# Kernel optimization log

Hardware: AMD Instinct MI355X
Metric: run time of the kernel (lower is better)

## Reference

```python
import jax, jax.numpy as jnp
import numpy as np

B, T, C, H = 4, 2048, 1024, 16
HS = C // H  # head dim = 64
EPS = 1e-5


def _layernorm(h, w, b):
    m = jnp.mean(h, axis=-1, keepdims=True)
    v = jnp.mean(jnp.square(h - m), axis=-1, keepdims=True)
    return (h - m) * jax.lax.rsqrt(v + EPS) * w + b


def _quantize_int8(t):
    # per-tensor absmax int8 quantization, matching the torch code
    absmax = jnp.max(jnp.abs(t))
    scale = jnp.where(absmax > 0, absmax / 127.0, jnp.float32(1.0))
    q = jnp.clip(jnp.round(t / scale), -127, 127).astype(jnp.int8)
    return q, scale


def setup_inputs() -> dict:
    key = jax.random.key(0)
    ks = jax.random.split(key, 8)
    w = lambda k, shape: (jax.random.normal(k, shape, jnp.float32) * 0.02)
    return {
        "x": jax.random.normal(ks[0], (B, T, C), jnp.float32),
        "ln1_w": jnp.ones((C,), jnp.float32),
        "ln1_b": jnp.zeros((C,), jnp.float32),
        "W_qkv": w(ks[1], (C, 3 * C)),
        "b_qkv": jnp.zeros((3 * C,), jnp.float32),
        "W_o": w(ks[2], (C, C)),
        "b_o": jnp.zeros((C,), jnp.float32),
        "ln2_w": jnp.ones((C,), jnp.float32),
        "ln2_b": jnp.zeros((C,), jnp.float32),
        "W_fc": w(ks[3], (C, 4 * C)),
        "b_fc": jnp.zeros((4 * C,), jnp.float32),
        "W_pr": w(ks[4], (4 * C, C)),
        "b_pr": jnp.zeros((C,), jnp.float32),
    }


def reference(x, ln1_w, ln1_b, W_qkv, b_qkv, W_o, b_o, ln2_w, ln2_b, W_fc, b_fc, W_pr, b_pr):
    # ---- attention (prefill, cache-owner, kv_cache_quant=True, use_cache=True) ----
    h = _layernorm(x, ln1_w, ln1_b)
    qkv = h @ W_qkv + b_qkv                       # (B,T,3C)
    q, k, v = jnp.split(qkv, 3, axis=-1)
    q = q.reshape(B, T, H, HS).transpose(0, 2, 1, 3)  # (B,H,T,hs)
    k = k.reshape(B, T, H, HS).transpose(0, 2, 1, 3)
    v = v.reshape(B, T, H, HS).transpose(0, 2, 1, 3)

    # quantized `present` cache (returned, not used for attention in prefill path)
    k_quant, k_scale = _quantize_int8(k)
    v_quant, v_scale = _quantize_int8(v)

    # causal SDPA (dropout=0)
    att = jnp.einsum("bhqd,bhkd->bhqk", q, k) * (1.0 / np.sqrt(HS))
    causal = jnp.tril(jnp.ones((T, T), bool))
    att = jnp.where(causal[None, None], att, jnp.float32(-jnp.inf))
    att = jax.nn.softmax(att, axis=-1)
    y = jnp.einsum("bhqk,bhkd->bhqd", att, v)
    y = y.transpose(0, 2, 1, 3).reshape(B, T, C)
    y = y @ W_o + b_o
    x = x + y

    # ---- MLP ----
    h2 = _layernorm(x, ln2_w, ln2_b)
    h2 = jax.nn.gelu(h2 @ W_fc + b_fc, approximate=False)
    x = x + (h2 @ W_pr + b_pr)

    return x, k_quant, k_scale, v_quant, v_scale
```

## Files before the change

kernel.cpp:

```cpp
#include <hip/hip_runtime.h>
#include <cmath>

typedef __bf16 bf16;
typedef float f32x4 __attribute__((ext_vector_type(4)));
typedef __bf16 bf16x4 __attribute__((ext_vector_type(4)));
typedef __bf16 bf16x8 __attribute__((ext_vector_type(8)));

#define DEVI __device__ __forceinline__

constexpr int Bn = 4, Tn = 2048, Cn = 1024, Hn = 16, HSn = 64;
constexpr int C3n = 3 * Cn;
constexpr int BTn = Bn * Tn;

constexpr size_t OFF_WT_QKV = 0;
constexpr size_t OFF_WT_O   = 6291456;
constexpr size_t OFF_WT_FC  = 8388608;
constexpr size_t OFF_WT_PR  = 16777216;
constexpr size_t OFF_H      = 25165824;
constexpr size_t OFF_Y      = 41943040;
constexpr size_t OFF_X1     = 58720256;
constexpr size_t OFF_AMAX   = 92274688;
constexpr size_t OFF_QKV    = 92274944;
constexpr size_t OFF_G      = OFF_QKV;

constexpr size_t OUT_X  = 0;
constexpr size_t OUT_KQ = 8388608;
constexpr size_t OUT_KS = 16777216;
constexpr size_t OUT_VQ = 16777217;
constexpr size_t OUT_VS = 25165825;

DEVI void g2l16(const void* g, void* l) {
  __builtin_amdgcn_global_load_lds(
      (__attribute__((address_space(1))) void*)g,
      (__attribute__((address_space(3))) void*)l, 16, 0, 0);
}

DEVI float gelu_f(float x) {
  const float ax = fabsf(x) * 0.7071067811865476f;
  const float t = 1.0f / (1.0f + 0.3275911f * ax);
  const float p = t * (0.254829592f + t * (-0.284496736f +
                  t * (1.421413741f + t * (-1.453152027f + t * 1.061405429f))));
  float er = 1.0f - p * __expf(-ax * ax);
  er = (x < 0.0f) ? -er : er;
  return 0.5f * x * (1.0f + er);
}

__global__ __launch_bounds__(256) void k_transpose(const float* __restrict__ W,
                                                   bf16* __restrict__ Wt,
                                                   int K, int N) {
  __shared__ float tile[32][33];
  const int n0 = blockIdx.x * 32, k0 = blockIdx.y * 32;
  const int tx = threadIdx.x, ty = threadIdx.y;
#pragma unroll
  for (int i = 0; i < 4; ++i) {
    int k = k0 + ty + i * 8;
    tile[ty + i * 8][tx] = W[(size_t)k * N + (n0 + tx)];
  }
  __syncthreads();
#pragma unroll
  for (int i = 0; i < 4; ++i) {
    int n = n0 + ty + i * 8;
    Wt[(size_t)n * K + (k0 + tx)] = (bf16)tile[tx][ty + i * 8];
  }
}

__global__ __launch_bounds__(256) void k_ln(const float* __restrict__ x,
                                            const float* __restrict__ g,
                                            const float* __restrict__ b,
                                            bf16* __restrict__ out) {
  __shared__ float red[8];
  const int row = blockIdx.x, tid = threadIdx.x;
  const int lane = tid & 63, wv = tid >> 6;
  f32x4 v = ((const f32x4*)(x + (size_t)row * Cn))[tid];

  float s = v[0] + v[1] + v[2] + v[3];
  s += __shfl_down(s, 32); s += __shfl_down(s, 16); s += __shfl_down(s, 8);
  s += __shfl_down(s, 4);  s += __shfl_down(s, 2);  s += __shfl_down(s, 1);
  if (!lane) red[wv] = s;
  __syncthreads();
  const float mean = (red[0] + red[1] + red[2] + red[3]) * (1.0f / 1024.0f);
  __syncthreads();

  f32x4 d = v - mean;
  float s2 = d[0]*d[0] + d[1]*d[1] + d[2]*d[2] + d[3]*d[3];
  s2 += __shfl_down(s2, 32); s2 += __shfl_down(s2, 16); s2 += __shfl_down(s2, 8);
  s2 += __shfl_down(s2, 4);  s2 += __shfl_down(s2, 2);  s2 += __shfl_down(s2, 1);
  if (!lane) red[wv] = s2;
  __syncthreads();
  const float var = (red[0] + red[1] + red[2] + red[3]) * (1.0f / 1024.0f);
  const float inv = rsqrtf(var + 1e-5f);

  f32x4 gw = ((const f32x4*)g)[tid];
  f32x4 bb = ((const f32x4*)b)[tid];
  bf16x4 o;
#pragma unroll
  for (int j = 0; j < 4; ++j) o[j] = (bf16)(d[j] * inv * gw[j] + bb[j]);
  *(bf16x4*)(out + (size_t)row * Cn + tid * 4) = o;
}

#define VMCNT(N) asm volatile("s_waitcnt vmcnt(" #N ")" ::: "memory")
#define LGKM0()  asm volatile("s_waitcnt lgkmcnt(0)" ::: "memory")
#define BARW()   asm volatile("s_barrier" ::: "memory")
#define SCHEDB() __builtin_amdgcn_sched_barrier(0)

DEVI void stage_half(const bf16* __restrict__ G, int ldk, int row0, int k0,
                     bf16* dst, int w, int lane) {
  const int srow = lane >> 3;
  const int sch = ((lane & 7) ^ srow) * 8;
  const bf16* src = G + (size_t)(row0 + srow) * ldk + k0 + sch;
#pragma unroll
  for (int i = 0; i < 2; ++i) {
    const int g = 2 * w + i;
    g2l16(src + (size_t)(8 * g) * ldk, dst + g * 512);
  }
}

DEVI void read_b(const bf16* BsB, int wn, int l15, int quad, bf16x8 (&bv)[2][2]) {
#pragma unroll
  for (int nt = 0; nt < 2; ++nt)
#pragma unroll
    for (int kk = 0; kk < 2; ++kk) {
      const int row = wn * 32 + nt * 16 + l15;
      const int c = ((kk * 4 + quad) ^ (l15 & 7)) * 8;
      bv[nt][kk] = *(const bf16x8*)(BsB + row * 64 + c);
    }
}

template <int Q>
DEVI void read_aq(const bf16* AsB, int wm, int l15, int quad, bf16x8 (&af)[2]) {
#pragma unroll
  for (int kk = 0; kk < 2; ++kk) {
    const int row = wm * 64 + Q * 16 + l15;
    const int c = ((kk * 4 + quad) ^ (l15 & 7)) * 8;
    af[kk] = *(const bf16x8*)(AsB + row * 64 + c);
  }
}

template <int Q>
DEVI void mfma_q(const bf16x8 (&af)[2], const bf16x8 (&bv)[2][2],
                 f32x4 (&acc)[4][2]) {
  __builtin_amdgcn_s_setprio(1);
#pragma unroll
  for (int nt = 0; nt < 2; ++nt)
#pragma unroll
    for (int kk = 0; kk < 2; ++kk)
      acc[Q][nt] = __builtin_amdgcn_mfma_f32_16x16x32_bf16(
          af[kk], bv[nt][kk], acc[Q][nt], 0, 0, 0);
  __builtin_amdgcn_s_setprio(0);
}

template <int BUF>
DEVI void tile_iter(int kt, int kIters, const bf16* __restrict__ A,
                    const bf16* __restrict__ Bt, int K, int m0, int n0,
                    bf16* As0, bf16* As1, bf16* Bs0, bf16* Bs1,
                    f32x4 (&acc)[4][2], int w, int lane) {
  const int l15 = lane & 15, quad = lane >> 4;
  const int wm = w >> 2, wn = w & 3;
  const bf16* AsB = BUF ? As1 : As0;
  const bf16* BsB = BUF ? Bs1 : Bs0;
  bf16* AsW = BUF ? As1 : As0;
  bf16* BsW = BUF ? Bs1 : Bs0;

  bf16x8 bv[2][2];
  bf16x8 af0[2], af1[2], af2[2], af3[2];

  read_b(BsB, wn, l15, quad, bv);
  read_aq<0>(AsB, wm, l15, quad, af0);
  read_aq<1>(AsB, wm, l15, quad, af1);
  LGKM0(); SCHEDB();
  mfma_q<0>(af0, bv, acc);
  SCHEDB();

  read_aq<2>(AsB, wm, l15, quad, af2);
  read_aq<3>(AsB, wm, l15, quad, af3);
  LGKM0(); SCHEDB();
  mfma_q<1>(af1, bv, acc);
  SCHEDB();
  BARW();

  if (kt + 2 < kIters) {
    stage_half(A,  K, m0, (kt + 2) * 64, AsW, w, lane);
    stage_half(Bt, K, n0, (kt + 2) * 64, BsW, w, lane);
  }
  mfma_q<2>(af2, bv, acc);
  mfma_q<3>(af3, bv, acc);
  SCHEDB();
  if (kt + 2 < kIters) {
    VMCNT(4);
    BARW();
  } else if (kt + 1 < kIters) {
    VMCNT(0);
    BARW();
  }
}

template <bool RES, bool GELU, bool AMAX, bool F32OUT>
__global__ __launch_bounds__(512, 4) void k_gemmT(const bf16* __restrict__ A,
                                                  const bf16* __restrict__ Bt,
                                                  const float* __restrict__ bias,
                                                  const float* __restrict__ res,
                                                  void* __restrict__ Cout,
                                                  unsigned int* __restrict__ amax,
                                                  int M, int N, int K) {
  __shared__ bf16 As0[128 * 64], As1[128 * 64];
  __shared__ bf16 Bs0[128 * 64], Bs1[128 * 64];
  __shared__ float redA[8];
  const int tid = threadIdx.x;
  const int lane = tid & 63, w = tid >> 6;
  const int wm = w >> 2, wn = w & 3;
  const int l15 = lane & 15, quad = lane >> 4;
  const int m0 = blockIdx.x * 128, n0 = blockIdx.y * 128;
  const int kIters = K >> 6;
  (void)M;

  stage_half(A,  K, m0, 0,  As0, w, lane);
  stage_half(Bt, K, n0, 0,  Bs0, w, lane);
  stage_half(A,  K, m0, 64, As1, w, lane);
  stage_half(Bt, K, n0, 64, Bs1, w, lane);
  VMCNT(4);
  BARW();

  f32x4 acc[4][2] = {};

  const int nPairs = kIters >> 1;
  for (int p = 0; p < nPairs; ++p) {
    tile_iter<0>(2 * p,     kIters, A, Bt, K, m0, n0, As0, As1, Bs0, Bs1, acc, w, lane);
    tile_iter<1>(2 * p + 1, kIters, A, Bt, K, m0, n0, As0, As1, Bs0, Bs1, acc, w, lane);
  }

  const int colB = n0 + wn * 32 + l15;
  const int rowB = m0 + wm * 64 + (quad << 2);
  float lm = 0.0f;
#pragma unroll
  for (int mt = 0; mt < 4; ++mt) {
#pragma unroll
    for (int nt = 0; nt < 2; ++nt) {
      const int col = colB + nt * 16;
      const float bval = bias[col];
#pragma unroll
      for (int r = 0; r < 4; ++r) {
        const int row = rowB + mt * 16 + r;
        float val = acc[mt][nt][r] + bval;
        if (GELU) val = gelu_f(val);
        if (RES)  val += res[(size_t)row * N + col];
        if (AMAX) lm = fmaxf(lm, fabsf(val));
        if (F32OUT) ((float*)Cout)[(size_t)row * N + col] = val;
        else        ((bf16*)Cout)[(size_t)row * N + col] = (bf16)val;
      }
    }
  }

  if (AMAX) {
    const int cls = n0 >> 10;
    if (cls > 0) {
      lm = fmaxf(lm, __shfl_xor(lm, 1));
      lm = fmaxf(lm, __shfl_xor(lm, 2));
      lm = fmaxf(lm, __shfl_xor(lm, 4));
      lm = fmaxf(lm, __shfl_xor(lm, 8));
      lm = fmaxf(lm, __shfl_xor(lm, 16));
      lm = fmaxf(lm, __shfl_xor(lm, 32));
      if (!lane) redA[w] = lm;
      __syncthreads();
      if (tid == 0) {
        float m8 = redA[0];
#pragma unroll
        for (int i = 1; i < 8; ++i) m8 = fmaxf(m8, redA[i]);
        atomicMax(amax + (cls - 1), __float_as_uint(m8));
      }
    }
  }
}

__global__ __launch_bounds__(256) void k_init(unsigned int* amax) {
  if (threadIdx.x < 2) amax[threadIdx.x] = 0u;
}

__global__ __launch_bounds__(256) void k_quant(const bf16* __restrict__ qkv,
                                               const unsigned int* __restrict__ amax,
                                               float* __restrict__ out) {
  const float ka = __uint_as_float(amax[0]);
  const float va = __uint_as_float(amax[1]);
  const float ks = ka > 0.0f ? ka / 127.0f : 1.0f;
  const float vs = va > 0.0f ? va / 127.0f : 1.0f;
  if (blockIdx.x == 0 && threadIdx.x == 0) { out[OUT_KS] = ks; out[OUT_VS] = vs; }
  const float kinv = 1.0f / ks, vinv = 1.0f / vs;
  const size_t nchunks = 1048576;
  const size_t stride = (size_t)gridDim.x * blockDim.x;
  for (size_t ci = (size_t)blockIdx.x * blockDim.x + threadIdx.x; ci < nchunks; ci += stride) {
    const int d0 = (int)(ci & 7) * 8;
    const int t  = (int)(ci >> 3) & 2047;
    const int h  = (int)(ci >> 14) & 15;
    const int b  = (int)(ci >> 18);
    const size_t src = ((size_t)(b * Tn + t)) * C3n + h * HSn + d0;
    bf16x8 k8 = *(const bf16x8*)(qkv + src + Cn);
    bf16x8 v8 = *(const bf16x8*)(qkv + src + 2 * Cn);
    float kq[8], vq[8];
#pragma unroll
    for (int j = 0; j < 8; ++j) {
      kq[j] = fminf(fmaxf(rintf((float)k8[j] * kinv), -127.0f), 127.0f);
      vq[j] = fminf(fmaxf(rintf((float)v8[j] * vinv), -127.0f), 127.0f);
    }
    const size_t oi = ci * 8;
    f32x4 a0 = {kq[0], kq[1], kq[2], kq[3]};
    f32x4 a1 = {kq[4], kq[5], kq[6], kq[7]};
    *(f32x4*)(out + OUT_KQ + oi)     = a0;
    *(f32x4*)(out + OUT_KQ + oi + 4) = a1;
    float* vdst = out + OUT_VQ + oi;
#pragma unroll
    for (int j = 0; j < 8; ++j) vdst[j] = vq[j];
  }
}

__global__ __launch_bounds__(256, 3) void k_attn(const bf16* __restrict__ qkv,
                                                 bf16* __restrict__ y) {
  __shared__ bf16 Ks[2][64 * 64];
  __shared__ bf16 Vt[2][64 * 64];
  __shared__ bf16 Pt[4][2][16 * 64];

  const int tid = threadIdx.x;
  const int lane = tid & 63;
  const int w = tid >> 6;
  const int quad = lane >> 4;
  const int l15 = lane & 15;

  const int bh = blockIdx.x;
  const int qt = 15 - (int)blockIdx.y;
  const int b = bh >> 4, h = bh & 15;
  const int q0 = qt * 128;
  const int ktMax = 2 * qt + 1;

  const bf16* qkv_b = qkv + (size_t)b * Tn * C3n + h * HSn;
  const bf16* kbase = qkv_b + Cn;
  const bf16* vbase = qkv_b + 2 * Cn;

  const int srow = lane >> 3;
  const int schunk = ((lane & 7) ^ srow) * 8;

  const bf16* q0p = qkv_b + (size_t)(q0 + 16 * w + l15) * C3n;
  const bf16* q1p = q0p + (size_t)64 * C3n;
  bf16x8 qf[2][2];
  qf[0][0] = *(const bf16x8*)(q0p + quad * 8);
  qf[0][1] = *(const bf16x8*)(q0p + 32 + quad * 8);
  qf[1][0] = *(const bf16x8*)(q1p + quad * 8);
  qf[1][1] = *(const bf16x8*)(q1p + 32 + quad * 8);

  g2l16(kbase + (size_t)(8 * w + srow) * C3n + schunk, (bf16*)Ks[0] + w * 512);
  g2l16(kbase + (size_t)(8 * (w + 4) + srow) * C3n + schunk, (bf16*)Ks[0] + (w + 4) * 512);
  bf16x8 v0 = *(const bf16x8*)(vbase + (size_t)lane * C3n + w * 8);
  bf16x8 v1 = *(const bf16x8*)(vbase + (size_t)lane * C3n + (w + 4) * 8);
  __builtin_amdgcn_s_waitcnt(0);
#pragma unroll
  for (int j = 0; j < 8; ++j) {
    Vt[0][(w * 8 + j) * 64 + ((srow ^ j) << 3) + (lane & 7)] = v0[j];
    Vt[0][((w + 4) * 8 + j) * 64 + ((srow ^ j) << 3) + (lane & 7)] = v1[j];
  }
  __syncthreads();

  f32x4 Od[2][4] = {};
  float m_i[2] = {-INFINITY, -INFINITY};
  float l_i[2] = {0.0f, 0.0f};

  for (int kt = 0; kt <= ktMax; ++kt) {
    const int bsel = kt & 1;

    bf16x8 nv0, nv1;
    if (kt < ktMax) {
      const int kv1 = (kt + 1) * 64;
      g2l16(kbase + (size_t)(kv1 + 8 * w + srow) * C3n + schunk,
            (bf16*)Ks[bsel ^ 1] + w * 512);
      g2l16(kbase + (size_t)(kv1 + 8 * (w + 4) + srow) * C3n + schunk,
            (bf16*)Ks[bsel ^ 1] + (w + 4) * 512);
      nv0 = *(const bf16x8*)(vbase + (size_t)(kv1 + lane) * C3n + w * 8);
      nv1 = *(const bf16x8*)(vbase + (size_t)(kv1 + lane) * C3n + (w + 4) * 8);
    }

    const bf16* KsB = Ks[bsel];
    f32x4 S0[4] = {}, S1[4] = {};
#pragma unroll
    for (int ks = 0; ks < 2; ++ks)
#pragma unroll
      for (int nt = 0; nt < 4; ++nt) {
        const int rn = nt * 16 + l15;
        const int c = ((ks * 4 + quad) ^ (l15 & 7)) * 8;
        bf16x8 kf = *(const bf16x8*)(KsB + rn * 64 + c);
        S0[nt] = __builtin_amdgcn_mfma_f32_16x16x32_bf16(kf, qf[0][ks], S0[nt], 0, 0, 0);
        S1[nt] = __builtin_amdgcn_mfma_f32_16x16x32_bf16(kf, qf[1][ks], S1[nt], 0, 0, 0);
      }

    const int qloc = 16 * w + l15;
    const int th[2] = { kt < 2 * qt ? 64 : (kt == 2 * qt ? qloc : -1),
                        kt < ktMax ? 64 : qloc };
    f32x4* Sg[2] = {S0, S1};
#pragma unroll
    for (int g = 0; g < 2; ++g) {
      float s[4][4];
      float mx = -INFINITY;
#pragma unroll
      for (int nt = 0; nt < 4; ++nt)
#pragma unroll
        for (int r = 0; r < 4; ++r) {
          float v = Sg[g][nt][r] * 0.125f;
          if (nt * 16 + quad * 4 + r > th[g]) v = -INFINITY;
          s[nt][r] = v;
          mx = fmaxf(mx, v);
        }
      mx = fmaxf(mx, __shfl_xor(mx, 16));
      mx = fmaxf(mx, __shfl_xor(mx, 32));
      const float mn = fmaxf(m_i[g], mx);
      const float al = __expf(m_i[g] - mn);
      m_i[g] = mn;
      float rsum = 0.0f;
      bf16x4 pk[4];
#pragma unroll
      for (int nt = 0; nt < 4; ++nt)
#pragma unroll
        for (int r = 0; r < 4; ++r) {
          const float p = __expf(s[nt][r] - mn);
          rsum += p;
          pk[nt][r] = (bf16)p;
        }
      rsum += __shfl_xor(rsum, 16);
      rsum += __shfl_xor(rsum, 32);
      l_i[g] = l_i[g] * al + rsum;
#pragma unroll
      for (int dt = 0; dt < 4; ++dt) Od[g][dt] *= al;
#pragma unroll
      for (int nt = 0; nt < 4; ++nt) {
        const int phys = (nt * 2 + (quad >> 1)) ^ (l15 & 7);
        *(bf16x4*)(&Pt[w][g][0] + l15 * 64 + phys * 8 + (quad & 1) * 4) = pk[nt];
      }
    }

    const bf16* VtB = Vt[bsel];
#pragma unroll
    for (int ks2 = 0; ks2 < 2; ++ks2) {
      const int pc = ((ks2 * 4 + quad) ^ (l15 & 7)) * 8;
      bf16x8 pf0 = *(const bf16x8*)(&Pt[w][0][0] + l15 * 64 + pc);
      bf16x8 pf1 = *(const bf16x8*)(&Pt[w][1][0] + l15 * 64 + pc);
#pragma unroll
      for (int dt = 0; dt < 4; ++dt) {
        const int d = dt * 16 + l15;
        bf16x8 vf = *(const bf16x8*)(VtB + d * 64 + pc);
        Od[0][dt] = __builtin_amdgcn_mfma_f32_16x16x32_bf16(vf, pf0, Od[0][dt], 0, 0, 0);
        Od[1][dt] = __builtin_amdgcn_mfma_f32_16x16x32_bf16(vf, pf1, Od[1][dt], 0, 0, 0);
      }
    }

    if (kt < ktMax) {
      __builtin_amdgcn_s_waitcnt(0);
#pragma unroll
      for (int j = 0; j < 8; ++j) {
        Vt[bsel ^ 1][(w * 8 + j) * 64 + ((srow ^ j) << 3) + (lane & 7)] = nv0[j];
        Vt[bsel ^ 1][((w + 4) * 8 + j) * 64 + ((srow ^ j) << 3) + (lane & 7)] = nv1[j];
      }
      __syncthreads();
    }
  }

#pragma unroll
  for (int g = 0; g < 2; ++g) {
    const float invl = 1.0f / l_i[g];
    const size_t yb = ((size_t)b * Tn + q0 + g * 64 + 16 * w + l15) * Cn + h * HSn;
#pragma unroll
    for (int dt = 0; dt < 4; ++dt) {
      bf16x4 o;
#pragma unroll
      for (int r = 0; r < 4; ++r) o[r] = (bf16)(Od[g][dt][r] * invl);
      *(bf16x4*)(y + yb + dt * 16 + quad * 4) = o;
    }
  }
}

extern "C" void kernel_launch(void* const* d_in, const int* in_sizes, int n_in,
                              void* d_out, int out_size, void* d_ws, size_t ws_size,
                              hipStream_t stream) {
  const float* x     = (const float*)d_in[0];
  const float* ln1w  = (const float*)d_in[1];
  const float* ln1b  = (const float*)d_in[2];
  const float* Wqkv  = (const float*)d_in[3];
  const float* bqkv  = (const float*)d_in[4];
  const float* Wo    = (const float*)d_in[5];
  const float* bo    = (const float*)d_in[6];
  const float* ln2w  = (const float*)d_in[7];
  const float* ln2b  = (const float*)d_in[8];
  const float* Wfc   = (const float*)d_in[9];
  const float* bfc   = (const float*)d_in[10];
  const float* Wpr   = (const float*)d_in[11];
  const float* bpr   = (const float*)d_in[12];

  char* ws = (char*)d_ws;
  bf16*  Wt_qkv = (bf16*)(ws + OFF_WT_QKV);
  bf16*  Wt_o   = (bf16*)(ws + OFF_WT_O);
  bf16*  Wt_fc  = (bf16*)(ws + OFF_WT_FC);
  bf16*  Wt_pr  = (bf16*)(ws + OFF_WT_PR);
  bf16*  h      = (bf16*)(ws + OFF_H);
  bf16*  ybf    = (bf16*)(ws + OFF_Y);
  float* x1     = (float*)(ws + OFF_X1);
  unsigned int* amax = (unsigned int*)(ws + OFF_AMAX);
  bf16*  qkvbf  = (bf16*)(ws + OFF_QKV);
  bf16*  g      = (bf16*)(ws + OFF_G);
  float* out    = (float*)d_out;

  const dim3 tb(32, 8);
  k_transpose<<<dim3(96, 32),  tb, 0, stream>>>(Wqkv, Wt_qkv, 1024, 3072);
  k_transpose<<<dim3(32, 32),  tb, 0, stream>>>(Wo,   Wt_o,   1024, 1024);
  k_transpose<<<dim3(128, 32), tb, 0, stream>>>(Wfc,  Wt_fc,  1024, 4096);
  k_transpose<<<dim3(32, 128), tb, 0, stream>>>(Wpr,  Wt_pr,  4096, 1024);
  k_init<<<1, 64, 0, stream>>>(amax);

  k_ln<<<BTn, 256, 0, stream>>>(x, ln1w, ln1b, h);
  k_gemmT<false, false, true, false><<<dim3(64, 24), 512, 0, stream>>>(
      h, Wt_qkv, bqkv, nullptr, qkvbf, amax, 8192, 3072, 1024);
  k_quant<<<2048, 256, 0, stream>>>(qkvbf, amax, out);
  k_attn<<<dim3(64, 16), 256, 0, stream>>>(qkvbf, ybf);
  k_gemmT<true, false, false, true><<<dim3(64, 8), 512, 0, stream>>>(
      ybf, Wt_o, bo, x, x1, nullptr, 8192, 1024, 1024);
  k_ln<<<BTn, 256, 0, stream>>>(x1, ln2w, ln2b, h);
  k_gemmT<false, true, false, false><<<dim3(64, 32), 512, 0, stream>>>(
      h, Wt_fc, bfc, nullptr, g, nullptr, 8192, 4096, 1024);
  k_gemmT<true, false, false, true><<<dim3(64, 8), 512, 0, stream>>>(
      g, Wt_pr, bpr, x1, out, nullptr, 8192, 1024, 4096);
}
```

Baseline: 527.1 us.

## Merge weight transposes and amax init into one launch; relax GEMM MFMA scheduling

The four weight-transpose kernels and the amax-init kernel become one k_prep launch that picks each block's job by block index, removing four launches and the small gaps between them. Separately, the GEMM inner loop loses its sched_barrier fences, the s_setprio raise around MFMA groups and the intermediate lgkmcnt wait. All four A fragments are now read before any MFMA and the compiler schedules freely. This may raise register pressure or lose the hand-tuned overlap of LDS reads with MFMAs.

```diff
diff --git a/kernel.cpp b/kernel.cpp
--- a/kernel.cpp
+++ b/kernel.cpp
@@ -45,11 +45,24 @@
   return 0.5f * x * (1.0f + er);
 }
 
-__global__ __launch_bounds__(256) void k_transpose(const float* __restrict__ W,
-                                                   bf16* __restrict__ Wt,
-                                                   int K, int N) {
+struct TrJob { const float* W; bf16* Wt; int K, N, bx; };
+
+__global__ __launch_bounds__(256) void k_prep(const float* W0, bf16* T0,
+                                              const float* W1, bf16* T1,
+                                              const float* W2, bf16* T2,
+                                              const float* W3, bf16* T3,
+                                              unsigned int* amax) {
   __shared__ float tile[32][33];
-  const int n0 = blockIdx.x * 32, k0 = blockIdx.y * 32;
+  const int id = blockIdx.x;
+  if (id == 0 && threadIdx.x == 0 && threadIdx.y == 0) { amax[0] = 0u; amax[1] = 0u; }
+
+  const float* W; bf16* Wt; int K, N, lid;
+  if (id < 3072)      { W = W0; Wt = T0; K = 1024; N = 3072; lid = id; }
+  else if (id < 4096) { W = W1; Wt = T1; K = 1024; N = 1024; lid = id - 3072; }
+  else if (id < 8192) { W = W2; Wt = T2; K = 1024; N = 4096; lid = id - 4096; }
+  else                { W = W3; Wt = T3; K = 4096; N = 1024; lid = id - 8192; }
+  const int gx = N >> 5;
+  const int n0 = (lid % gx) * 32, k0 = (lid / gx) * 32;
   const int tx = threadIdx.x, ty = threadIdx.y;
 #pragma unroll
   for (int i = 0; i < 4; ++i) {
@@ -101,7 +114,6 @@
 #define VMCNT(N) asm volatile("s_waitcnt vmcnt(" #N ")" ::: "memory")
 #define LGKM0()  asm volatile("s_waitcnt lgkmcnt(0)" ::: "memory")
 #define BARW()   asm volatile("s_barrier" ::: "memory")
-#define SCHEDB() __builtin_amdgcn_sched_barrier(0)
 
 DEVI void stage_half(const bf16* __restrict__ G, int ldk, int row0, int k0,
                      bf16* dst, int w, int lane) {
@@ -139,14 +151,12 @@
 template <int Q>
 DEVI void mfma_q(const bf16x8 (&af)[2], const bf16x8 (&bv)[2][2],
                  f32x4 (&acc)[4][2]) {
-  __builtin_amdgcn_s_setprio(1);
 #pragma unroll
   for (int nt = 0; nt < 2; ++nt)
 #pragma unroll
     for (int kk = 0; kk < 2; ++kk)
       acc[Q][nt] = __builtin_amdgcn_mfma_f32_16x16x32_bf16(
           af[kk], bv[nt][kk], acc[Q][nt], 0, 0, 0);
-  __builtin_amdgcn_s_setprio(0);
 }
 
 template <int BUF>
@@ -167,15 +177,12 @@
   read_b(BsB, wn, l15, quad, bv);
   read_aq<0>(AsB, wm, l15, quad, af0);
   read_aq<1>(AsB, wm, l15, quad, af1);
-  LGKM0(); SCHEDB();
-  mfma_q<0>(af0, bv, acc);
-  SCHEDB();
-
   read_aq<2>(AsB, wm, l15, quad, af2);
   read_aq<3>(AsB, wm, l15, quad, af3);
-  LGKM0(); SCHEDB();
+  mfma_q<0>(af0, bv, acc);
   mfma_q<1>(af1, bv, acc);
-  SCHEDB();
+
+  LGKM0();
   BARW();
 
   if (kt + 2 < kIters) {
@@ -184,7 +191,6 @@
   }
   mfma_q<2>(af2, bv, acc);
   mfma_q<3>(af3, bv, acc);
-  SCHEDB();
   if (kt + 2 < kIters) {
     VMCNT(4);
     BARW();
@@ -269,10 +275,6 @@
       }
     }
   }
-}
-
-__global__ __launch_bounds__(256) void k_init(unsigned int* amax) {
-  if (threadIdx.x < 2) amax[threadIdx.x] = 0u;
 }
 
 __global__ __launch_bounds__(256) void k_quant(const bf16* __restrict__ qkv,
@@ -501,12 +503,8 @@
   bf16*  g      = (bf16*)(ws + OFF_G);
   float* out    = (float*)d_out;
 
-  const dim3 tb(32, 8);
-  k_transpose<<<dim3(96, 32),  tb, 0, stream>>>(Wqkv, Wt_qkv, 1024, 3072);
-  k_transpose<<<dim3(32, 32),  tb, 0, stream>>>(Wo,   Wt_o,   1024, 1024);
-  k_transpose<<<dim3(128, 32), tb, 0, stream>>>(Wfc,  Wt_fc,  1024, 4096);
-  k_transpose<<<dim3(32, 128), tb, 0, stream>>>(Wpr,  Wt_pr,  4096, 1024);
-  k_init<<<1, 64, 0, stream>>>(amax);
+  k_prep<<<dim3(12288), dim3(32, 8), 0, stream>>>(Wqkv, Wt_qkv, Wo, Wt_o,
+                                                  Wfc, Wt_fc, Wpr, Wt_pr, amax);
 
   k_ln<<<BTn, 256, 0, stream>>>(x, ln1w, ln1b, h);
   k_gemmT<false, false, true, false><<<dim3(64, 24), 512, 0, stream>>>(
```

Result: no change. 523.0 us (-0.8%).
